# Performance work log

Hardware: AMD Instinct MI355X
Metric: run time of the kernel (lower is better)

The kernel has to match this reference:

```python
import jax, jax.numpy as jnp
import numpy as np

B, N = 4, 65536
Z_DIM, HIDDEN, N_LAYERS = 64, 128, 4
PE_FREQS = 10
FEAT_RES = 16  # global_feat_res
IN_DIM = Z_DIM + 3 + 3 * 2 * PE_FREQS  # latent + pos-encoded coords


def setup_inputs() -> dict:
    key = jax.random.key(0)
    ks = jax.random.split(key, 4 + 2 * N_LAYERS)
    inp = {}
    # xyz in [-1,1]: used directly as grid_sample grid coordinates
    inp['xyz'] = jax.random.uniform(ks[0], (B, N, 3), jnp.float32, -1.0, 1.0)
    inp['local_latents'] = jax.random.normal(ks[1], (B, Z_DIM, FEAT_RES, FEAT_RES), jnp.float32)
    dims = [IN_DIM] + [HIDDEN] * N_LAYERS
    for i in range(N_LAYERS):
        inp[f'W{i}'] = jax.random.normal(ks[2 + i], (dims[i], dims[i + 1]), jnp.float32) / np.sqrt(dims[i]).astype(np.float32)
        inp[f'b{i}'] = jnp.zeros((dims[i + 1],), jnp.float32)
    inp['Wa'] = jax.random.normal(ks[2 + N_LAYERS], (HIDDEN, 1), jnp.float32) / np.sqrt(HIDDEN).astype(np.float32)
    inp['ba'] = jnp.zeros((1,), jnp.float32)
    return inp


def grid_sample_2d(img, grid):
    # torch F.grid_sample: bilinear, align_corners=False, padding_mode='zeros'
    # img [B,C,H,W], grid [B,Hg,Wg,2] in [-1,1], (x,y) order -> out [B,C,Hg,Wg]
    _, _, H, W = img.shape
    x = (grid[..., 0] + 1.0) * (W * 0.5) - 0.5
    y = (grid[..., 1] + 1.0) * (H * 0.5) - 0.5
    x0 = jnp.floor(x); y0 = jnp.floor(y)
    x1 = x0 + 1.0; y1 = y0 + 1.0

    def gather(ix, iy):
        valid = (ix >= 0) & (ix <= W - 1) & (iy >= 0) & (iy <= H - 1)
        ixc = jnp.clip(ix, 0, W - 1).astype(jnp.int32)
        iyc = jnp.clip(iy, 0, H - 1).astype(jnp.int32)
        v = jax.vmap(lambda im, yy, xx: im[:, yy, xx])(img, iyc, ixc)  # [B,C,Hg,Wg]
        return v * valid[:, None].astype(img.dtype)

    out = (gather(x0, y0) * ((x1 - x) * (y1 - y))[:, None]
           + gather(x0, y1) * ((x1 - x) * (y - y0))[:, None]
           + gather(x1, y0) * ((x - x0) * (y1 - y))[:, None]
           + gather(x1, y1) * ((x - x0) * (y - y0))[:, None])
    return out


def positional_encoding(x):
    # x [P,3] -> [P, 3 + 3*2*PE_FREQS]
    freqs = 2.0 ** jnp.arange(PE_FREQS, dtype=x.dtype)
    ang = x[..., None, :] * freqs[:, None]  # [P, L, 3]
    P = x.shape[0]
    return jnp.concatenate([x, jnp.sin(ang).reshape(P, -1), jnp.cos(ang).reshape(P, -1)], axis=-1)


def _forward(xyz, local_latents, Ws, bs, Wa, ba):
    xyz4 = xyz[:, None]  # [B, 1, N, 3] (forward's xyz.unsqueeze(1))
    # sample_local_latents: 4D latents -> grid = xyz[..., [0, 2]]
    grid = jnp.stack([xyz4[..., 0], xyz4[..., 2]], axis=-1)  # [B,1,N,2]
    samp = grid_sample_2d(local_latents, grid)               # [B,C,1,N]
    z = samp.transpose(0, 2, 3, 1).reshape(-1, Z_DIM)        # [B*N, C]
    # get_local_coordinates (preserve_y=True since latents are 4D)
    lc = (xyz4 + 1.0) * 0.5 * FEAT_RES
    lc = lc - jnp.round(lc - 0.5)  # round-half-to-even matches torch .round()
    lc = lc * 2.0 - 1.0
    coords = jnp.concatenate([lc[..., 0:1], xyz4[..., 1:2], lc[..., 2:3]], axis=-1).reshape(-1, 3)
    # local_generator MLP (viewdirs=None on alpha-only path)
    h = jnp.concatenate([z, positional_encoding(coords)], axis=-1)
    for W, b in zip(Ws, bs):
        h = jax.nn.relu(h @ W + b)
    alpha = h @ Wa + ba  # [B*N, 1], raw alpha (activation happens in volume render, not here)
    return alpha.reshape(xyz.shape[0], 1, -1)  # alpha.view(B, n_samples=1, samples_per_ray=N)


def reference(xyz, local_latents, W0, b0, W1, b1, W2, b2, W3, b3, Wa, ba):
    return _forward(xyz, local_latents, (W0, W1, W2, W3), (b0, b1, b2, b3), Wa, ba)
```

## Files before the change

kernel.cpp:

```cpp
#include <hip/hip_runtime.h>
#include <hip/hip_bf16.h>

typedef float f32x4 __attribute__((ext_vector_type(4)));
typedef short bf16x8 __attribute__((ext_vector_type(8)));

__device__ __forceinline__ unsigned pk2(float lo, float hi) {
  union { __hip_bfloat162 h2; unsigned u; } c;
  c.h2 = __float22bfloat162_rn(make_float2(lo, hi));
  return c.u;
}
__device__ __forceinline__ ushort f2bf1(float f) {
  union { __hip_bfloat16 h; ushort u; } c;
  c.h = __float2bfloat16(f);
  return c.u;
}
__device__ __forceinline__ float u2f(unsigned u) {
  union { unsigned u; float f; } c; c.u = u; return c.f;
}

__global__ void pack_all(const float* __restrict__ W0, const float* __restrict__ W1,
                         const float* __restrict__ W2, const float* __restrict__ W3,
                         const float* __restrict__ b0, const float* __restrict__ b1,
                         const float* __restrict__ b2, const float* __restrict__ b3,
                         const float* __restrict__ lat,
                         ushort* __restrict__ wpk, float* __restrict__ biasf,
                         ushort* __restrict__ latpk) {
  int t = blockIdx.x * 256 + threadIdx.x;
  if (t < 8192) {
    int lane = t & 63, kt = (t >> 6) & 3, jt = (t >> 8) & 7, layer = t >> 11;
    const float* W = layer == 0 ? W0 : layer == 1 ? W1 : layer == 2 ? W2 : W3;
    int K = (layer == 0) ? 127 : 128;
    int g = lane >> 4, r = lane & 15;
    bf16x8 pk;
#pragma unroll
    for (int i = 0; i < 8; i++) {
      int k = kt * 32 + 8 * g + i;
      pk[i] = (short)((k < K) ? f2bf1(W[k * 128 + jt * 16 + r]) : (ushort)0);
    }
    *(bf16x8*)(wpk + (((t >> 11) * 32 + (jt * 4 + kt)) * 64 + lane) * 8) = pk;
  } else if (t < 16384) {
    int t2 = t - 8192;
    int g = t2 & 7, pix = (t2 >> 3) & 255, b = t2 >> 11;
    uint4 w;
    unsigned* wp = &w.x;
#pragma unroll
    for (int i = 0; i < 4; i++)
      wp[i] = pk2(lat[(b * 64 + 8 * g + 2 * i) * 256 + pix],
                  lat[(b * 64 + 8 * g + 2 * i + 1) * 256 + pix]);
    *(uint4*)((char*)latpk + b * 32768 + pix * 128 + ((16 * g) ^ ((pix & 7) << 4))) = w;
  } else if (t < 16896) {
    int t3 = t - 16384;
    int layer = t3 >> 7, j = t3 & 127;
    const float* b = layer == 0 ? b0 : layer == 1 ? b1 : layer == 2 ? b2 : b3;
    biasf[t3] = b[j];
  }
}

__global__ __launch_bounds__(256, 2) void scene_fwd(
    const float* __restrict__ xyz, const ushort* __restrict__ latpk,
    const ushort* __restrict__ wpk, const float* __restrict__ biasf,
    const float* __restrict__ wa, const float* __restrict__ ba,
    float* __restrict__ out) {
  __shared__ char smem[65536];
  const int tid = threadIdx.x;
  const int wave = tid >> 6, lane = tid & 63;
  const int g = lane >> 4, r = lane & 15;
  const int p0 = blockIdx.x * 256 + wave * 64;
  const int batch = blockIdx.x >> 8;

  {
    uint4* dst = (uint4*)smem;
    const uint4* src = (const uint4*)((const char*)latpk + batch * 32768);
#pragma unroll
    for (int i = 0; i < 8; i++) dst[i * 256 + tid] = src[i * 256 + tid];
  }
  __syncthreads();

  const int p = p0 + lane;
  const float X = xyz[3 * p + 0], Y = xyz[3 * p + 1], Z = xyz[3 * p + 2];
  uint4 fr[8];
  uint4 fe[8];
  {
    float gx = (X + 1.f) * 8.f - 0.5f;
    float gy = (Z + 1.f) * 8.f - 0.5f;
    float x0f = floorf(gx), y0f = floorf(gy);
    float fx = gx - x0f, fy = gy - y0f;
    int ix0 = (int)x0f, iy0 = (int)y0f;
    int ix1 = ix0 + 1, iy1 = iy0 + 1;
    float vx0 = (ix0 >= 0 && ix0 <= 15) ? 1.f : 0.f;
    float vx1 = (ix1 >= 0 && ix1 <= 15) ? 1.f : 0.f;
    float vy0 = (iy0 >= 0 && iy0 <= 15) ? 1.f : 0.f;
    float vy1 = (iy1 >= 0 && iy1 <= 15) ? 1.f : 0.f;
    int cx0 = min(max(ix0, 0), 15), cx1 = min(max(ix1, 0), 15);
    int cy0 = min(max(iy0, 0), 15), cy1 = min(max(iy1, 0), 15);
    float w00 = (1.f - fx) * (1.f - fy) * vx0 * vy0;
    float w01 = (1.f - fx) * fy * vx0 * vy1;
    float w10 = fx * (1.f - fy) * vx1 * vy0;
    float w11 = fx * fy * vx1 * vy1;
    int px00 = cy0 * 16 + cx0, px01 = cy1 * 16 + cx0;
    int px10 = cy0 * 16 + cx1, px11 = cy1 * 16 + cx1;
    int o00 = px00 * 128, s00 = (px00 & 7) << 4;
    int o01 = px01 * 128, s01 = (px01 & 7) << 4;
    int o10 = px10 * 128, s10 = (px10 & 7) << 4;
    int o11 = px11 * 128, s11 = (px11 & 7) << 4;
#pragma unroll
    for (int gr = 0; gr < 8; gr++) {
      const int off = 16 * gr;
      uint4 c00 = *(const uint4*)(smem + o00 + (off ^ s00));
      uint4 c01 = *(const uint4*)(smem + o01 + (off ^ s01));
      uint4 c10 = *(const uint4*)(smem + o10 + (off ^ s10));
      uint4 c11 = *(const uint4*)(smem + o11 + (off ^ s11));
      const unsigned* u00 = &c00.x; const unsigned* u01 = &c01.x;
      const unsigned* u10 = &c10.x; const unsigned* u11 = &c11.x;
      unsigned* wo = &fr[gr].x;
#pragma unroll
      for (int q = 0; q < 4; q++) {
        float lo = w00 * u2f(u00[q] << 16) + w01 * u2f(u01[q] << 16) +
                   w10 * u2f(u10[q] << 16) + w11 * u2f(u11[q] << 16);
        float hi = w00 * u2f(u00[q] & 0xffff0000u) + w01 * u2f(u01[q] & 0xffff0000u) +
                   w10 * u2f(u10[q] & 0xffff0000u) + w11 * u2f(u11[q] & 0xffff0000u);
        wo[q] = pk2(lo, hi);
      }
    }
    float feat[64];
    float lcx = (X + 1.f) * 8.f; lcx = lcx - rintf(lcx - 0.5f); lcx = lcx * 2.f - 1.f;
    float lcz = (Z + 1.f) * 8.f; lcz = lcz - rintf(lcz - 0.5f); lcz = lcz * 2.f - 1.f;
    feat[0] = lcx; feat[1] = Y; feat[2] = lcz;
    const float cc[3] = {lcx, Y, lcz};
#pragma unroll
    for (int f = 0; f < 10; f++) {
      const float s = (float)(1 << f);
#pragma unroll
      for (int d = 0; d < 3; d++) {
        feat[3 + 3 * f + d]  = __sinf(cc[d] * s);
        feat[33 + 3 * f + d] = __cosf(cc[d] * s);
      }
    }
    feat[63] = 0.f;
#pragma unroll
    for (int gr = 0; gr < 8; gr++) {
      unsigned* wo = &fe[gr].x;
#pragma unroll
      for (int q = 0; q < 4; q++)
        wo[q] = pk2(feat[8 * gr + 2 * q], feat[8 * gr + 2 * q + 1]);
    }
  }
  __syncthreads();

  char* hb = smem + wave * 16384;
  {
    char* rowp = hb + lane * 256;
    const unsigned swz = (unsigned)((lane & 7) << 4);
#pragma unroll
    for (int gr = 0; gr < 8; gr++)
      *(uint4*)(rowp + (((unsigned)(16 * gr)) ^ swz)) = fr[gr];
#pragma unroll
    for (int gr = 0; gr < 8; gr++)
      *(uint4*)(rowp + (((unsigned)(128 + 16 * gr)) ^ swz)) = fe[gr];
  }

  f32x4 acc[8][4];
#pragma unroll 1
  for (int layer = 0; layer < 4; layer++) {
    const float* bias = biasf + layer * 128;
    const ushort* Aw = wpk + layer * 16384;
#pragma unroll
    for (int jt = 0; jt < 8; jt++) {
      f32x4 bf = *(const f32x4*)(bias + jt * 16 + 4 * g);
#pragma unroll
      for (int pt = 0; pt < 4; pt++) acc[jt][pt] = bf;
    }
#pragma unroll
    for (int kt = 0; kt < 4; kt++) {
      bf16x8 Bf[4];
#pragma unroll
      for (int pt = 0; pt < 4; pt++) {
        const int pr = pt * 16 + r;
        Bf[pt] = *(const bf16x8*)(hb + pr * 256 +
                  (((unsigned)(kt * 64 + 16 * g)) ^ ((unsigned)((pr & 7) << 4))));
      }
#pragma unroll
      for (int jt = 0; jt < 8; jt++) {
        bf16x8 Af = *(const bf16x8*)(Aw + ((jt * 4 + kt) * 64 + lane) * 8);
#pragma unroll
        for (int pt = 0; pt < 4; pt++)
          acc[jt][pt] = __builtin_amdgcn_mfma_f32_16x16x32_bf16(Af, Bf[pt], acc[jt][pt], 0, 0, 0);
      }
    }
    if (layer < 3) {
#pragma unroll
      for (int jt = 0; jt < 8; jt++) {
#pragma unroll
        for (int pt = 0; pt < 4; pt++) {
          const int pr = pt * 16 + r;
          uint2 w;
          w.x = pk2(fmaxf(acc[jt][pt][0], 0.f), fmaxf(acc[jt][pt][1], 0.f));
          w.y = pk2(fmaxf(acc[jt][pt][2], 0.f), fmaxf(acc[jt][pt][3], 0.f));
          *(uint2*)(hb + pr * 256 +
                    (((unsigned)(32 * jt + 8 * g)) ^ ((unsigned)((pr & 7) << 4)))) = w;
        }
      }
    }
  }
  const float ba0 = ba[0];
  float part[4] = {0.f, 0.f, 0.f, 0.f};
#pragma unroll
  for (int jt = 0; jt < 8; jt++) {
    f32x4 wf = *(const f32x4*)(wa + jt * 16 + 4 * g);
#pragma unroll
    for (int pt = 0; pt < 4; pt++) {
#pragma unroll
      for (int i = 0; i < 4; i++)
        part[pt] += fmaxf(acc[jt][pt][i], 0.f) * wf[i];
    }
  }
#pragma unroll
  for (int pt = 0; pt < 4; pt++) {
    float s = part[pt];
    s += __shfl_xor(s, 16, 64);
    s += __shfl_xor(s, 32, 64);
    if (lane < 16) out[p0 + pt * 16 + lane] = s + ba0;
  }
}

extern "C" void kernel_launch(void* const* d_in, const int* in_sizes, int n_in,
                              void* d_out, int out_size, void* d_ws, size_t ws_size,
                              hipStream_t stream) {
  const float* xyz = (const float*)d_in[0];
  const float* lat = (const float*)d_in[1];
  const float* W0 = (const float*)d_in[2];
  const float* b0 = (const float*)d_in[3];
  const float* W1 = (const float*)d_in[4];
  const float* b1 = (const float*)d_in[5];
  const float* W2 = (const float*)d_in[6];
  const float* b2 = (const float*)d_in[7];
  const float* W3 = (const float*)d_in[8];
  const float* b3 = (const float*)d_in[9];
  const float* wa = (const float*)d_in[10];
  const float* ba = (const float*)d_in[11];
  float* out = (float*)d_out;
  ushort* wpk = (ushort*)d_ws;
  float* biasf = (float*)((char*)d_ws + 131072);
  ushort* latpk = (ushort*)((char*)d_ws + 139264);

  pack_all<<<66, 256, 0, stream>>>(W0, W1, W2, W3, b0, b1, b2, b3, lat,
                                   wpk, biasf, latpk);
  scene_fwd<<<1024, 256, 0, stream>>>(xyz, latpk, wpk, biasf, wa, ba, out);
}
```

Baseline: 62.06 us.

## Split MLP N-dimension across wave pairs and halve block size for occupancy

Each block now handles 128 points instead of 256. Pairs of waves share one 64-row activation tile, and each wave computes half of the 128 output columns, so the accumulator array shrinks from 8x4 to 4x4. The input features are also split: half the threads do the bilinear latent sampling and the other half do the positional encoding. Shared memory drops to 32KB and launch bounds target 4 blocks per CU, trading lower register pressure and higher occupancy for extra block-wide barriers per layer and a cross-wave reduction for the final alpha dot product.

```diff
diff --git a/kernel.cpp b/kernel.cpp
--- a/kernel.cpp
+++ b/kernel.cpp
@@ -37,7 +37,7 @@
       int k = kt * 32 + 8 * g + i;
       pk[i] = (short)((k < K) ? f2bf1(W[k * 128 + jt * 16 + r]) : (ushort)0);
     }
-    *(bf16x8*)(wpk + (((t >> 11) * 32 + (jt * 4 + kt)) * 64 + lane) * 8) = pk;
+    *(bf16x8*)(wpk + ((t >> 11) * 32 + (jt * 4 + kt)) * 512 + lane * 8) = pk;
   } else if (t < 16384) {
     int t2 = t - 8192;
     int g = t2 & 7, pix = (t2 >> 3) & 255, b = t2 >> 11;
@@ -56,17 +56,17 @@
   }
 }
 
-__global__ __launch_bounds__(256, 2) void scene_fwd(
+__global__ __launch_bounds__(256, 4) void scene_fwd(
     const float* __restrict__ xyz, const ushort* __restrict__ latpk,
     const ushort* __restrict__ wpk, const float* __restrict__ biasf,
     const float* __restrict__ wa, const float* __restrict__ ba,
     float* __restrict__ out) {
-  __shared__ char smem[65536];
+  __shared__ char smem[32768];
   const int tid = threadIdx.x;
   const int wave = tid >> 6, lane = tid & 63;
   const int g = lane >> 4, r = lane & 15;
-  const int p0 = blockIdx.x * 256 + wave * 64;
-  const int batch = blockIdx.x >> 8;
+  const int p0 = blockIdx.x * 128;
+  const int batch = blockIdx.x >> 9;
 
   {
     uint4* dst = (uint4*)smem;
@@ -76,11 +76,11 @@
   }
   __syncthreads();
 
-  const int p = p0 + lane;
+  const int t2 = tid & 127;
+  const int p = p0 + t2;
   const float X = xyz[3 * p + 0], Y = xyz[3 * p + 1], Z = xyz[3 * p + 2];
   uint4 fr[8];
-  uint4 fe[8];
-  {
+  if (tid < 128) {
     float gx = (X + 1.f) * 8.f - 0.5f;
     float gy = (Z + 1.f) * 8.f - 0.5f;
     float x0f = floorf(gx), y0f = floorf(gy);
@@ -106,67 +106,84 @@
 #pragma unroll
     for (int gr = 0; gr < 8; gr++) {
       const int off = 16 * gr;
-      uint4 c00 = *(const uint4*)(smem + o00 + (off ^ s00));
-      uint4 c01 = *(const uint4*)(smem + o01 + (off ^ s01));
-      uint4 c10 = *(const uint4*)(smem + o10 + (off ^ s10));
-      uint4 c11 = *(const uint4*)(smem + o11 + (off ^ s11));
-      const unsigned* u00 = &c00.x; const unsigned* u01 = &c01.x;
-      const unsigned* u10 = &c10.x; const unsigned* u11 = &c11.x;
-      unsigned* wo = &fr[gr].x;
-#pragma unroll
-      for (int q = 0; q < 4; q++) {
-        float lo = w00 * u2f(u00[q] << 16) + w01 * u2f(u01[q] << 16) +
-                   w10 * u2f(u10[q] << 16) + w11 * u2f(u11[q] << 16);
-        float hi = w00 * u2f(u00[q] & 0xffff0000u) + w01 * u2f(u01[q] & 0xffff0000u) +
-                   w10 * u2f(u10[q] & 0xffff0000u) + w11 * u2f(u11[q] & 0xffff0000u);
-        wo[q] = pk2(lo, hi);
-      }
-    }
-    float feat[64];
+      float f[8];
+#pragma unroll
+      for (int i = 0; i < 8; i++) f[i] = 0.f;
+#pragma unroll
+      for (int c = 0; c < 4; c++) {
+        const char* ap = smem + (c == 0 ? o00 + (off ^ s00) : c == 1 ? o01 + (off ^ s01)
+                               : c == 2 ? o10 + (off ^ s10) : o11 + (off ^ s11));
+        const float wc = c == 0 ? w00 : c == 1 ? w01 : c == 2 ? w10 : w11;
+        uint4 cv = *(const uint4*)ap;
+        const unsigned* u = &cv.x;
+#pragma unroll
+        for (int q = 0; q < 4; q++) {
+          f[2 * q]     += wc * u2f(u[q] << 16);
+          f[2 * q + 1] += wc * u2f(u[q] & 0xffff0000u);
+        }
+      }
+      fr[gr].x = pk2(f[0], f[1]); fr[gr].y = pk2(f[2], f[3]);
+      fr[gr].z = pk2(f[4], f[5]); fr[gr].w = pk2(f[6], f[7]);
+    }
+  } else {
     float lcx = (X + 1.f) * 8.f; lcx = lcx - rintf(lcx - 0.5f); lcx = lcx * 2.f - 1.f;
     float lcz = (Z + 1.f) * 8.f; lcz = lcz - rintf(lcz - 0.5f); lcz = lcz * 2.f - 1.f;
-    feat[0] = lcx; feat[1] = Y; feat[2] = lcz;
-    const float cc[3] = {lcx, Y, lcz};
-#pragma unroll
-    for (int f = 0; f < 10; f++) {
-      const float s = (float)(1 << f);
-#pragma unroll
-      for (int d = 0; d < 3; d++) {
-        feat[3 + 3 * f + d]  = __sinf(cc[d] * s);
-        feat[33 + 3 * f + d] = __cosf(cc[d] * s);
-      }
-    }
-    feat[63] = 0.f;
+    const float c0 = lcx, c1 = Y, c2 = lcz;
 #pragma unroll
     for (int gr = 0; gr < 8; gr++) {
-      unsigned* wo = &fe[gr].x;
-#pragma unroll
-      for (int q = 0; q < 4; q++)
-        wo[q] = pk2(feat[8 * gr + 2 * q], feat[8 * gr + 2 * q + 1]);
-    }
-  }
-  __syncthreads();
-
-  char* hb = smem + wave * 16384;
+      unsigned* wo = &fr[gr].x;
+#pragma unroll
+      for (int q = 0; q < 4; q++) {
+        float e[2];
+#pragma unroll
+        for (int h = 0; h < 2; h++) {
+          const int idx = 8 * gr + 2 * q + h;
+          float v;
+          if (idx == 0) v = c0;
+          else if (idx == 1) v = c1;
+          else if (idx == 2) v = c2;
+          else if (idx == 63) v = 0.f;
+          else if (idx < 33) {
+            const int s = idx - 3;
+            const int d = s % 3;
+            const float cc = d == 0 ? c0 : d == 1 ? c1 : c2;
+            v = __sinf(cc * (float)(1 << (s / 3)));
+          } else {
+            const int s = idx - 33;
+            const int d = s % 3;
+            const float cc = d == 0 ? c0 : d == 1 ? c1 : c2;
+            v = __cosf(cc * (float)(1 << (s / 3)));
+          }
+          e[h] = v;
+        }
+        wo[q] = pk2(e[0], e[1]);
+      }
+    }
+  }
+  __syncthreads();
+
   {
-    char* rowp = hb + lane * 256;
-    const unsigned swz = (unsigned)((lane & 7) << 4);
+    const int tile = t2 >> 6, row = t2 & 63;
+    char* rowp = smem + tile * 16384 + row * 256;
+    const unsigned swz = (unsigned)((row & 7) << 4);
+    const int base = (tid < 128) ? 0 : 128;
 #pragma unroll
     for (int gr = 0; gr < 8; gr++)
-      *(uint4*)(rowp + (((unsigned)(16 * gr)) ^ swz)) = fr[gr];
-#pragma unroll
-    for (int gr = 0; gr < 8; gr++)
-      *(uint4*)(rowp + (((unsigned)(128 + 16 * gr)) ^ swz)) = fe[gr];
-  }
-
-  f32x4 acc[8][4];
+      *(uint4*)(rowp + (((unsigned)(base + 16 * gr)) ^ swz)) = fr[gr];
+  }
+  __syncthreads();
+
+  const int tileM = wave >> 1;
+  const int jh = wave & 1;
+  char* hb = smem + tileM * 16384;
+  f32x4 acc[4][4];
 #pragma unroll 1
   for (int layer = 0; layer < 4; layer++) {
     const float* bias = biasf + layer * 128;
     const ushort* Aw = wpk + layer * 16384;
 #pragma unroll
-    for (int jt = 0; jt < 8; jt++) {
-      f32x4 bf = *(const f32x4*)(bias + jt * 16 + 4 * g);
+    for (int jt = 0; jt < 4; jt++) {
+      f32x4 bf = *(const f32x4*)(bias + (jh * 4 + jt) * 16 + 4 * g);
 #pragma unroll
       for (int pt = 0; pt < 4; pt++) acc[jt][pt] = bf;
     }
@@ -180,16 +197,17 @@
                   (((unsigned)(kt * 64 + 16 * g)) ^ ((unsigned)((pr & 7) << 4))));
       }
 #pragma unroll
-      for (int jt = 0; jt < 8; jt++) {
-        bf16x8 Af = *(const bf16x8*)(Aw + ((jt * 4 + kt) * 64 + lane) * 8);
+      for (int jt = 0; jt < 4; jt++) {
+        bf16x8 Af = *(const bf16x8*)(Aw + ((jh * 4 + jt) * 4 + kt) * 512 + lane * 8);
 #pragma unroll
         for (int pt = 0; pt < 4; pt++)
           acc[jt][pt] = __builtin_amdgcn_mfma_f32_16x16x32_bf16(Af, Bf[pt], acc[jt][pt], 0, 0, 0);
       }
     }
+    __syncthreads();
     if (layer < 3) {
 #pragma unroll
-      for (int jt = 0; jt < 8; jt++) {
+      for (int jt = 0; jt < 4; jt++) {
 #pragma unroll
         for (int pt = 0; pt < 4; pt++) {
           const int pr = pt * 16 + r;
@@ -197,16 +215,18 @@
           w.x = pk2(fmaxf(acc[jt][pt][0], 0.f), fmaxf(acc[jt][pt][1], 0.f));
           w.y = pk2(fmaxf(acc[jt][pt][2], 0.f), fmaxf(acc[jt][pt][3], 0.f));
           *(uint2*)(hb + pr * 256 +
-                    (((unsigned)(32 * jt + 8 * g)) ^ ((unsigned)((pr & 7) << 4)))) = w;
+                    (((unsigned)(32 * (jh * 4 + jt) + 8 * g)) ^ ((unsigned)((pr & 7) << 4)))) = w;
         }
       }
-    }
-  }
+      __syncthreads();
+    }
+  }
+
   const float ba0 = ba[0];
   float part[4] = {0.f, 0.f, 0.f, 0.f};
 #pragma unroll
-  for (int jt = 0; jt < 8; jt++) {
-    f32x4 wf = *(const f32x4*)(wa + jt * 16 + 4 * g);
+  for (int jt = 0; jt < 4; jt++) {
+    f32x4 wf = *(const f32x4*)(wa + (jh * 4 + jt) * 16 + 4 * g);
 #pragma unroll
     for (int pt = 0; pt < 4; pt++) {
 #pragma unroll
@@ -214,12 +234,22 @@
         part[pt] += fmaxf(acc[jt][pt][i], 0.f) * wf[i];
     }
   }
+  float* scr = (float*)smem;
 #pragma unroll
   for (int pt = 0; pt < 4; pt++) {
     float s = part[pt];
     s += __shfl_xor(s, 16, 64);
     s += __shfl_xor(s, 32, 64);
-    if (lane < 16) out[p0 + pt * 16 + lane] = s + ba0;
+    if (lane < 16) scr[(tileM * 2 + jh) * 64 + pt * 16 + lane] = s;
+  }
+  __syncthreads();
+  if (jh == 0 && lane < 16) {
+#pragma unroll
+    for (int pt = 0; pt < 4; pt++) {
+      const int idx = pt * 16 + lane;
+      out[p0 + tileM * 64 + idx] =
+          scr[(tileM * 2) * 64 + idx] + scr[(tileM * 2 + 1) * 64 + idx] + ba0;
+    }
   }
 }
 
@@ -245,5 +275,5 @@
 
   pack_all<<<66, 256, 0, stream>>>(W0, W1, W2, W3, b0, b1, b2, b3, lat,
                                    wpk, biasf, latpk);
-  scene_fwd<<<1024, 256, 0, stream>>>(xyz, latpk, wpk, biasf, wa, ba, out);
-}
+  scene_fwd<<<2048, 256, 0, stream>>>(xyz, latpk, wpk, biasf, wa, ba, out);
+}
```

Measured after the change: 56.68 us. -8.7%, faster.
